# Optimization experiments

Hardware: AMD Instinct MI355X
Metric: run time of the kernel (lower is better)

The kernel has to match this reference:

```python
import jax, jax.numpy as jnp
import numpy as np

B, T, C = 16, 2048, 64

def setup_inputs() -> dict:
    key = jax.random.key(0)
    x = jax.random.normal(key, (B, T, C), dtype=jnp.float32)
    # learned scalar params (as in build()): r_sigma init 0.01, margin init 0.0
    r_sigma = jnp.array([0.01], dtype=jnp.float32)
    margin = jnp.array([0.0], dtype=jnp.float32)
    return {"x": x, "r_sigma": r_sigma, "margin": margin}

def reference(x, r_sigma, margin):
    # Pairwise squared euclidean distances via the gram trick:
    # ||xi - xj||^2 = ||xi||^2 + ||xj||^2 - 2 xi.xj  (mathematically identical
    # to the original diff -> norm -> square, but avoids the (B,T,T,C) tensor
    # and the non-differentiable sqrt(0) on the diagonal).
    _, size, _ = x.shape
    sq = jnp.sum(x * x, axis=-1)                              # (B,T)
    gram = jnp.einsum('btc,bsc->bts', x, x)                   # (B,T,T)
    sqdist = jnp.maximum(sq[:, :, None] + sq[:, None, :] - 2.0 * gram, 0.0)
    # Gaussian kernel with learned inverse-bandwidth and margin
    Kmat = jnp.exp(-sqdist * r_sigma[0] + margin[0])          # (B,T,T)
    # off-diagonal mask (zero self-similarity)
    Kmat = Kmat * (1.0 - jnp.eye(size, dtype=x.dtype))
    # residual kernel attention: x + K @ x
    return x + jnp.einsum('bts,bsc->btc', Kmat, x)
```

## Files before the change

### kernel.cpp

```cpp
#include <hip/hip_runtime.h>
#include <stdint.h>
#include <stddef.h>

#define BB 16
#define TT 2048
#define CC 64
#define NT 16

typedef __attribute__((ext_vector_type(8))) short short8;
typedef __attribute__((ext_vector_type(4))) short s16x4;
typedef __attribute__((ext_vector_type(4))) float f32x4;
typedef __attribute__((ext_vector_type(16))) float f32x16;

#if defined(__has_builtin)
#if __has_builtin(__builtin_amdgcn_exp2f)
#define EXP2(x) __builtin_amdgcn_exp2f(x)
#else
#define EXP2(x) exp2f(x)
#endif
#else
#define EXP2(x) exp2f(x)
#endif

static __device__ __forceinline__ unsigned short f2bf(float f) {
  union { float f; unsigned int u; } v; v.f = f;
  unsigned int u = v.u;
  return (unsigned short)((u + 0x7FFFu + ((u >> 16) & 1u)) >> 16);
}

static __device__ __forceinline__ short8 pack_swap(
    float a0, float a1, float a2, float a3,
    float a4, float a5, float a6, float a7) {
  unsigned X, Z, Y, W;
  asm("v_cvt_pk_bf16_f32 %0, %1, %2" : "=v"(X) : "v"(a0), "v"(a1));
  asm("v_cvt_pk_bf16_f32 %0, %1, %2" : "=v"(Z) : "v"(a2), "v"(a3));
  asm("v_cvt_pk_bf16_f32 %0, %1, %2" : "=v"(Y) : "v"(a4), "v"(a5));
  asm("v_cvt_pk_bf16_f32 %0, %1, %2" : "=v"(W) : "v"(a6), "v"(a7));
  asm("v_permlane32_swap_b32 %0, %1" : "+v"(X), "+v"(Y));
  asm("v_permlane32_swap_b32 %0, %1" : "+v"(Z), "+v"(W));
  union { unsigned u[4]; short8 s; } u;
  u.u[0] = X; u.u[1] = Z; u.u[2] = Y; u.u[3] = W;
  return u.s;
}

__global__ __launch_bounds__(256, 4) void prep_kernel(
    const float* __restrict__ x, unsigned short* __restrict__ xb,
    unsigned short* __restrict__ xbT, float* __restrict__ sq)
{
  __shared__ unsigned short tile[16 * 68];
  const int b   = blockIdx.x >> 7;
  const int t0  = (blockIdx.x & 127) << 4;
  const int tid = threadIdx.x;
  const int r   = tid >> 4;
  const int cg  = tid & 15;
  const int c4  = cg * 4;

  const size_t idx = (size_t)(b * TT + t0 + r) * CC + c4;
  const f32x4 v = *(const f32x4*)(x + idx);
  float ssq = v[0]*v[0] + v[1]*v[1] + v[2]*v[2] + v[3]*v[3];

  s16x4 hv;
  hv[0] = (short)f2bf(v[0]); hv[1] = (short)f2bf(v[1]);
  hv[2] = (short)f2bf(v[2]); hv[3] = (short)f2bf(v[3]);
  *(s16x4*)(xb + idx) = hv;
  *(s16x4*)(&tile[r * 68 + c4]) = hv;

  ssq += __shfl_xor(ssq, 1); ssq += __shfl_xor(ssq, 2);
  ssq += __shfl_xor(ssq, 4); ssq += __shfl_xor(ssq, 8);
  if (cg == 0) sq[(size_t)b * TT + t0 + r] = ssq;
  __syncthreads();

  const int c = tid >> 2, tq = tid & 3;
  s16x4 o;
#pragma unroll
  for (int k = 0; k < 4; ++k) o[k] = (short)tile[(tq * 4 + k) * 68 + c];
  *(s16x4*)(xbT + (size_t)(b * CC + c) * TT + t0 + tq * 4) = o;
}

__global__ __launch_bounds__(512, 4) void attn_kernel(
    const float* __restrict__ x, const unsigned short* __restrict__ xb,
    const unsigned short* __restrict__ xbT, const float* __restrict__ sq,
    const float* __restrict__ rsig, const float* __restrict__ marg,
    float* __restrict__ out)
{
  __shared__ unsigned short SMEM[2][16384];
  __shared__ float SqLds[2][128];

  const int bid = ((blockIdx.x & 7) << 6) | (blockIdx.x >> 3);
  const int b   = bid >> 5;
  const int qb  = (bid & 31) << 6;
  const int tid = threadIdx.x;
  const int w = tid >> 6, lane = tid & 63;
  const int l31 = lane & 31, hi1 = lane >> 5;
  const int wq = w & 1, ws = w >> 1;

  const float L2E = 1.44269504088896f;
  const float rl2 = -rsig[0] * L2E;
  const float ml2 = marg[0] * L2E;

  const unsigned short* xb_b  = xb  + (size_t)b * TT * CC;
  const unsigned short* xbT_b = xbT + (size_t)b * CC * TT;
  const float* sq_b = sq + (size_t)b * TT;

  const int q0w = qb + wq * 32;

  short8 qf[4];
#pragma unroll
  for (int kc = 0; kc < 4; ++kc)
    qf[kc] = *(const short8*)(xb_b + (size_t)(q0w + l31) * CC + kc * 16 + hi1 * 8);
  const float aq = sq_b[q0w + l31];

  f32x16 oacc[2];
#pragma unroll
  for (int ct = 0; ct < 2; ++ct)
#pragma unroll
    for (int i = 0; i < 16; ++i) oacc[ct][i] = 0.f;

  const int srowK = tid >> 3, slotK = tid & 7;
  const int swzK  = srowK * 64 + ((slotK ^ (srowK & 7)) * 8);
  const int srowV = tid >> 4, slotV = tid & 15;
  const int swzV  = srowV * 128 + ((slotV ^ (srowV & 7)) * 8);

  short8 sK0, sK1, sV0, sV1;
  f32x4 sS;
  auto LOADT = [&](int t) {
    const size_t tb = (size_t)t * 128;
    sK0 = *(const short8*)(xb_b + (tb + srowK) * CC + slotK * 8);
    sK1 = *(const short8*)(xb_b + (tb + 64 + srowK) * CC + slotK * 8);
    sV0 = *(const short8*)(xbT_b + (size_t)srowV * TT + tb + slotV * 8);
    sV1 = *(const short8*)(xbT_b + (size_t)(srowV + 32) * TT + tb + slotV * 8);
    if (tid < 32) sS = *(const f32x4*)(sq_b + tb + tid * 4);
  };
  auto WRITET = [&](int bf) {
    unsigned short* Kp = &SMEM[bf][0];
    unsigned short* Vp = &SMEM[bf][8192];
    *(short8*)(&Kp[swzK])            = sK0;
    *(short8*)(&Kp[swzK + 64 * 64])  = sK1;
    *(short8*)(&Vp[swzV])            = sV0;
    *(short8*)(&Vp[swzV + 32 * 128]) = sV1;
    if (tid < 32) *(f32x4*)(&SqLds[bf][tid * 4]) = sS;
  };

  LOADT(0); WRITET(0);
  __syncthreads();

  const int rk = ws * 32 + l31;
  const int dQ = q0w - ws * 32;
  const int dtile  = dQ >> 7;
  const bool dvalid = ((dQ & 127) == 0) && dtile >= 0 && dtile < NT;

  for (int t = 0; t < NT; ++t) {
    const int cur = t & 1;
    if (t + 1 < NT) LOADT(t + 1);

    const unsigned short* Kp = &SMEM[cur][0];
    const unsigned short* Vp = &SMEM[cur][8192];

    f32x4 sqv[4];
#pragma unroll
    for (int ch = 0; ch < 4; ++ch)
      sqv[ch] = *(const f32x4*)(&SqLds[cur][ws * 32 + ch * 8 + 4 * hi1]);

    f32x16 sac;
#pragma unroll
    for (int i = 0; i < 16; ++i) sac[i] = 0.f;
#pragma unroll
    for (int kc = 0; kc < 4; ++kc) {
      const short8 kf = *(const short8*)(
          &Kp[rk * 64 + (((kc * 2 + hi1) ^ (rk & 7)) * 8)]);
      sac = __builtin_amdgcn_mfma_f32_32x32x16_bf16(kf, qf[kc], sac, 0, 0, 0);
    }

    float p[16];
#pragma unroll
    for (int r = 0; r < 16; ++r) {
      float d = fmaf(sac[r], -2.f, aq + sqv[r >> 2][r & 3]);
      d = fmaxf(d, 0.f);
      p[r] = EXP2(fmaf(d, rl2, ml2));
    }
    if (dvalid && t == dtile) {
#pragma unroll
      for (int r = 0; r < 16; ++r) {
        const int sl = (r & 3) + 8 * (r >> 2) + 4 * hi1;
        if (sl == l31) p[r] = 0.f;
      }
    }

    const short8 af0 = pack_swap(p[0], p[1], p[2],  p[3],  p[4],  p[5],  p[6],  p[7]);
    const short8 af1 = pack_swap(p[8], p[9], p[10], p[11], p[12], p[13], p[14], p[15]);

#pragma unroll
    for (int ct = 0; ct < 2; ++ct) {
      const int rc = ct * 32 + l31;
#pragma unroll
      for (int kk = 0; kk < 2; ++kk) {
        const short8 vf = *(const short8*)(
            &Vp[rc * 128 + (((ws * 4 + kk * 2 + hi1) ^ (rc & 7)) * 8)]);
        oacc[ct] = __builtin_amdgcn_mfma_f32_32x32x16_bf16(
            kk ? af1 : af0, vf, oacc[ct], 0, 0, 0);
      }
    }

    if (t + 1 < NT) WRITET(cur ^ 1);
    __syncthreads();
  }

  float* RedF = (float*)&SMEM[0][0];
  if (ws != 0) {
    const int base = ((ws - 1) * 2 + wq) * 2048;
#pragma unroll
    for (int ct = 0; ct < 2; ++ct)
#pragma unroll
      for (int r = 0; r < 16; ++r) {
        const int ql = (r & 3) + 8 * (r >> 2) + 4 * hi1;
        RedF[base + ql * 64 + ct * 32 + l31] = oacc[ct][r];
      }
  }
  __syncthreads();
  if (ws == 0) {
#pragma unroll
    for (int ct = 0; ct < 2; ++ct)
#pragma unroll
      for (int r = 0; r < 16; ++r) {
        const int ql = (r & 3) + 8 * (r >> 2) + 4 * hi1;
        const int c  = ct * 32 + l31;
        const int off = ql * 64 + c;
        const size_t idx = (size_t)(b * TT + qb + wq * 32 + ql) * CC + c;
        out[idx] = x[idx] + oacc[ct][r]
                 + RedF[(0 * 2 + wq) * 2048 + off]
                 + RedF[(1 * 2 + wq) * 2048 + off]
                 + RedF[(2 * 2 + wq) * 2048 + off];
      }
  }
}

extern "C" void kernel_launch(void* const* d_in, const int* in_sizes, int n_in,
                              void* d_out, int out_size, void* d_ws, size_t ws_size,
                              hipStream_t stream) {
  const float* x    = (const float*)d_in[0];
  const float* rsig = (const float*)d_in[1];
  const float* marg = (const float*)d_in[2];
  float* out = (float*)d_out;

  unsigned short* xb  = (unsigned short*)d_ws;
  unsigned short* xbT = xb + (size_t)BB * TT * CC;
  float* sq = (float*)(xbT + (size_t)BB * TT * CC);

  prep_kernel<<<2048, 256, 0, stream>>>(x, xb, xbT, sq);
  attn_kernel<<<512, 512, 0, stream>>>(x, xb, xbT, sq, rsig, marg, out);
}
```

Measured before the change: 110.0 us.

## Split QK accumulators, move LDS writes earlier, vectorize reduction epilogue, drop sq LDS

Several changes to the attention kernel. The squared-norm values are now read directly from global memory instead of being staged through LDS. The QK MFMA chain is split into two independent accumulators to shorten the dependency chain. The next-tile LDS write is moved before the PV MFMAs. The V swizzle now XORs with 16 slots instead of 8 to reduce bank conflicts. The epilogue has all waves write partials to LDS, then all threads do vectorized float4 reduction and output stores. These trade extra global loads and LDS traffic for more overlap and coalesced writes.

Measured after the change: 122.6 us. 1.12x slower.

```diff
diff --git a/kernel.cpp b/kernel.cpp
--- a/kernel.cpp
+++ b/kernel.cpp
@@ -84,7 +84,6 @@
     float* __restrict__ out)
 {
   __shared__ unsigned short SMEM[2][16384];
-  __shared__ float SqLds[2][128];
 
   const int bid = ((blockIdx.x & 7) << 6) | (blockIdx.x >> 3);
   const int b   = bid >> 5;
@@ -119,17 +118,15 @@
   const int srowK = tid >> 3, slotK = tid & 7;
   const int swzK  = srowK * 64 + ((slotK ^ (srowK & 7)) * 8);
   const int srowV = tid >> 4, slotV = tid & 15;
-  const int swzV  = srowV * 128 + ((slotV ^ (srowV & 7)) * 8);
+  const int swzV  = srowV * 128 + ((slotV ^ (srowV & 15)) * 8);
 
   short8 sK0, sK1, sV0, sV1;
-  f32x4 sS;
   auto LOADT = [&](int t) {
     const size_t tb = (size_t)t * 128;
     sK0 = *(const short8*)(xb_b + (tb + srowK) * CC + slotK * 8);
     sK1 = *(const short8*)(xb_b + (tb + 64 + srowK) * CC + slotK * 8);
     sV0 = *(const short8*)(xbT_b + (size_t)srowV * TT + tb + slotV * 8);
     sV1 = *(const short8*)(xbT_b + (size_t)(srowV + 32) * TT + tb + slotV * 8);
-    if (tid < 32) sS = *(const f32x4*)(sq_b + tb + tid * 4);
   };
   auto WRITET = [&](int bf) {
     unsigned short* Kp = &SMEM[bf][0];
@@ -138,7 +135,6 @@
     *(short8*)(&Kp[swzK + 64 * 64])  = sK1;
     *(short8*)(&Vp[swzV])            = sV0;
     *(short8*)(&Vp[swzV + 32 * 128]) = sV1;
-    if (tid < 32) *(f32x4*)(&SqLds[bf][tid * 4]) = sS;
   };
 
   LOADT(0); WRITET(0);
@@ -151,6 +147,7 @@
 
   for (int t = 0; t < NT; ++t) {
     const int cur = t & 1;
+    const int tb = t * 128;
     if (t + 1 < NT) LOADT(t + 1);
 
     const unsigned short* Kp = &SMEM[cur][0];
@@ -159,25 +156,33 @@
     f32x4 sqv[4];
 #pragma unroll
     for (int ch = 0; ch < 4; ++ch)
-      sqv[ch] = *(const f32x4*)(&SqLds[cur][ws * 32 + ch * 8 + 4 * hi1]);
-
-    f32x16 sac;
-#pragma unroll
-    for (int i = 0; i < 16; ++i) sac[i] = 0.f;
-#pragma unroll
-    for (int kc = 0; kc < 4; ++kc) {
-      const short8 kf = *(const short8*)(
-          &Kp[rk * 64 + (((kc * 2 + hi1) ^ (rk & 7)) * 8)]);
-      sac = __builtin_amdgcn_mfma_f32_32x32x16_bf16(kf, qf[kc], sac, 0, 0, 0);
+      sqv[ch] = *(const f32x4*)(sq_b + tb + ws * 32 + ch * 8 + 4 * hi1);
+
+    f32x16 sacA, sacB;
+#pragma unroll
+    for (int i = 0; i < 16; ++i) { sacA[i] = 0.f; sacB[i] = 0.f; }
+    {
+      const short8 kf0 = *(const short8*)(&Kp[rk * 64 + (((0 * 2 + hi1) ^ (rk & 7)) * 8)]);
+      const short8 kf1 = *(const short8*)(&Kp[rk * 64 + (((1 * 2 + hi1) ^ (rk & 7)) * 8)]);
+      const short8 kf2 = *(const short8*)(&Kp[rk * 64 + (((2 * 2 + hi1) ^ (rk & 7)) * 8)]);
+      const short8 kf3 = *(const short8*)(&Kp[rk * 64 + (((3 * 2 + hi1) ^ (rk & 7)) * 8)]);
+      sacA = __builtin_amdgcn_mfma_f32_32x32x16_bf16(kf0, qf[0], sacA, 0, 0, 0);
+      sacB = __builtin_amdgcn_mfma_f32_32x32x16_bf16(kf1, qf[1], sacB, 0, 0, 0);
+      sacA = __builtin_amdgcn_mfma_f32_32x32x16_bf16(kf2, qf[2], sacA, 0, 0, 0);
+      sacB = __builtin_amdgcn_mfma_f32_32x32x16_bf16(kf3, qf[3], sacB, 0, 0, 0);
     }
 
     float p[16];
 #pragma unroll
     for (int r = 0; r < 16; ++r) {
-      float d = fmaf(sac[r], -2.f, aq + sqv[r >> 2][r & 3]);
+      const float s2 = sacA[r] + sacB[r];
+      float d = fmaf(s2, -2.f, aq + sqv[r >> 2][r & 3]);
       d = fmaxf(d, 0.f);
       p[r] = EXP2(fmaf(d, rl2, ml2));
     }
+
+    if (t + 1 < NT) WRITET(cur ^ 1);
+
     if (dvalid && t == dtile) {
 #pragma unroll
       for (int r = 0; r < 16; ++r) {
@@ -195,19 +200,18 @@
 #pragma unroll
       for (int kk = 0; kk < 2; ++kk) {
         const short8 vf = *(const short8*)(
-            &Vp[rc * 128 + (((ws * 4 + kk * 2 + hi1) ^ (rc & 7)) * 8)]);
+            &Vp[rc * 128 + (((ws * 4 + kk * 2 + hi1) ^ (rc & 15)) * 8)]);
         oacc[ct] = __builtin_amdgcn_mfma_f32_32x32x16_bf16(
             kk ? af1 : af0, vf, oacc[ct], 0, 0, 0);
       }
     }
 
-    if (t + 1 < NT) WRITET(cur ^ 1);
     __syncthreads();
   }
 
   float* RedF = (float*)&SMEM[0][0];
-  if (ws != 0) {
-    const int base = ((ws - 1) * 2 + wq) * 2048;
+  {
+    const int base = w * 2048;
 #pragma unroll
     for (int ct = 0; ct < 2; ++ct)
 #pragma unroll
@@ -217,20 +221,19 @@
       }
   }
   __syncthreads();
-  if (ws == 0) {
-#pragma unroll
-    for (int ct = 0; ct < 2; ++ct)
-#pragma unroll
-      for (int r = 0; r < 16; ++r) {
-        const int ql = (r & 3) + 8 * (r >> 2) + 4 * hi1;
-        const int c  = ct * 32 + l31;
-        const int off = ql * 64 + c;
-        const size_t idx = (size_t)(b * TT + qb + wq * 32 + ql) * CC + c;
-        out[idx] = x[idx] + oacc[ct][r]
-                 + RedF[(0 * 2 + wq) * 2048 + off]
-                 + RedF[(1 * 2 + wq) * 2048 + off]
-                 + RedF[(2 * 2 + wq) * 2048 + off];
-      }
+
+#pragma unroll
+  for (int pass = 0; pass < 2; ++pass) {
+    const int q  = pass * 32 + (tid >> 4);
+    const int c4 = (tid & 15) * 4;
+    const int off = (q & 31) * 64 + c4;
+    f32x4 acc = *(const f32x4*)(&RedF[(0 * 2 + pass) * 2048 + off]);
+    acc += *(const f32x4*)(&RedF[(1 * 2 + pass) * 2048 + off]);
+    acc += *(const f32x4*)(&RedF[(2 * 2 + pass) * 2048 + off]);
+    acc += *(const f32x4*)(&RedF[(3 * 2 + pass) * 2048 + off]);
+    const size_t idx = (size_t)(b * TT + qb + q) * CC + c4;
+    const f32x4 xv = *(const f32x4*)(x + idx);
+    *(f32x4*)(out + idx) = acc + xv;
   }
 }
 
```
